# Optimization experiments

Measured on AMD Instinct MI355X. Metric: run time of the kernel, lower is better.

## Reference

```python
import jax, jax.numpy as jnp
import numpy as np
import math

NUM_BUCKETS = 32
MAX_DISTANCE = 128
EPS_IN = 1e-8
EPS_LN = 1e-5
NUM_HEADS = 12


def rms_inorm(x, w, eps=EPS_IN):
    # torch.std_mean default: unbiased (ddof=1) over spatial dims; mean is unused
    std = jnp.std(x, axis=(-2, -1), keepdims=True, ddof=1)
    return x / (std + eps) * w[None, :, None, None]


def layernorm(x, w, b, eps=EPS_LN):
    m = jnp.mean(x, axis=-1, keepdims=True)
    v = jnp.mean((x - m) ** 2, axis=-1, keepdims=True)
    return (x - m) * jax.lax.rsqrt(v + eps) * w + b


def _rel_bucket(rp):
    # T5-style bidirectional relative position buckets
    n = NUM_BUCKETS // 2
    ret = (rp > 0).astype(jnp.int32) * n
    arp = jnp.abs(rp)
    max_exact = n // 2
    is_small = arp < max_exact
    rpf = jnp.maximum(arp, 1).astype(jnp.float32)
    val_large = max_exact + (jnp.log(rpf / max_exact) / math.log(MAX_DISTANCE / max_exact) * (n - max_exact)).astype(jnp.int32)
    val_large = jnp.minimum(val_large, n - 1)
    return ret + jnp.where(is_small, arp, val_large)


def rel_bias(L, emb):
    pos = jnp.arange(L)
    bucket = _rel_bucket(pos[None, :] - pos[:, None])  # [L, L]
    return jnp.transpose(emb[bucket], (2, 0, 1))  # [heads, L, L]


def sdpa(q, k, v, bias):
    # q,k,v: [Bx, he, L, c]; bias: [he, L, L]
    scale = 1.0 / math.sqrt(q.shape[-1])
    s = jnp.einsum('bhlc,bhmc->bhlm', q, k) * scale + bias[None]
    p = jax.nn.softmax(s, axis=-1)
    return jnp.einsum('bhlm,bhmc->bhlc', p, v)


def _forward(x, norm1_w, norm2_w, mlpnorm_w, gamma_att, gamma_mlp,
             in_w, in_b, out_w, out_b, qn_w, qn_b, kn_w, kn_b,
             relbias_emb, mlp_w1, mlp_b1, mlp_w2, mlp_b2):
    B, C, H, W = x.shape
    he = NUM_HEADS
    hd = C // he
    inp = x
    x = rms_inorm(x, norm1_w)
    x = jnp.einsum('bchw,oc->bohw', x, in_w) + in_b[None, :, None, None]  # conv1x1 -> 3C
    x = x.reshape(B, he, 3 * hd, H, W).transpose(0, 1, 3, 4, 2)  # b he h w (3c)
    q, k, v = jnp.split(x, 3, axis=-1)
    q = layernorm(q, qn_w, qn_b)
    k = layernorm(k, kn_w, kn_b)
    # row attention: sequence along W
    to_x = lambda t: t.transpose(0, 2, 1, 3, 4).reshape(B * H, he, W, hd)
    xx = sdpa(to_x(q), to_x(k), to_x(v), rel_bias(W, relbias_emb))
    xx = xx.reshape(B, H, he, W, hd).transpose(0, 2, 4, 1, 3).reshape(B, C, H, W)
    # column attention: sequence along H
    to_y = lambda t: t.transpose(0, 3, 1, 2, 4).reshape(B * W, he, H, hd)
    xy = sdpa(to_y(q), to_y(k), to_y(v), rel_bias(H, relbias_emb))
    xy = xy.reshape(B, W, he, H, hd).transpose(0, 2, 4, 3, 1).reshape(B, C, H, W)
    x = (xx + xy) * 0.5
    x = rms_inorm(x, norm2_w)
    x = jnp.einsum('bchw,oc->bohw', x, out_w) + out_b[None, :, None, None]
    x = x * gamma_att[None, :, None, None] + inp
    inp2 = x
    h = x.transpose(0, 2, 3, 1)  # b h w c
    h = jax.nn.gelu(h @ mlp_w1 + mlp_b1, approximate=False) @ mlp_w2 + mlp_b2
    h = h.transpose(0, 3, 1, 2)
    h = rms_inorm(h, mlpnorm_w)
    return inp2 + gamma_mlp[None, :, None, None] * h


def setup_inputs() -> dict:
    key = jax.random.key(0)
    ks = jax.random.split(key, 8)
    B, C, H, W = 2, 768, 128, 128
    he = NUM_HEADS
    hd = C // he
    s = 0.02
    return {
        'x': jax.random.normal(ks[0], (B, C, H, W), jnp.float32),
        'bcs': jnp.zeros((B, 2), jnp.int32),
        'norm1_w': jnp.ones((C,), jnp.float32),
        'norm2_w': jnp.ones((C,), jnp.float32),
        'mlpnorm_w': jnp.ones((C,), jnp.float32),
        'gamma_att': jnp.full((C,), 1e-6, jnp.float32),
        'gamma_mlp': jnp.full((C,), 1e-6, jnp.float32),
        'in_w': jax.random.normal(ks[1], (3 * C, C), jnp.float32) * s,
        'in_b': jnp.zeros((3 * C,), jnp.float32),
        'out_w': jax.random.normal(ks[2], (C, C), jnp.float32) * s,
        'out_b': jnp.zeros((C,), jnp.float32),
        'qn_w': jnp.ones((hd,), jnp.float32),
        'qn_b': jnp.zeros((hd,), jnp.float32),
        'kn_w': jnp.ones((hd,), jnp.float32),
        'kn_b': jnp.zeros((hd,), jnp.float32),
        'relbias_emb': jax.random.normal(ks[3], (NUM_BUCKETS, he), jnp.float32) * s,
        'mlp_w1': jax.random.normal(ks[4], (C, 4 * C), jnp.float32) * s,
        'mlp_b1': jnp.zeros((4 * C,), jnp.float32),
        'mlp_w2': jax.random.normal(ks[5], (4 * C, C), jnp.float32) * s,
        'mlp_b2': jnp.zeros((C,), jnp.float32),
    }


def reference(x, bcs, norm1_w, norm2_w, mlpnorm_w, gamma_att, gamma_mlp,
              in_w, in_b, out_w, out_b, qn_w, qn_b, kn_w, kn_b,
              relbias_emb, mlp_w1, mlp_b1, mlp_w2, mlp_b2):
    # bcs is consulted only for boundary-condition selection in the original; the
    # T5-style relative bias here is independent of bc value.
    return _forward(x, norm1_w, norm2_w, mlpnorm_w, gamma_att, gamma_mlp,
                    in_w, in_b, out_w, out_b, qn_w, qn_b, kn_w, kn_b,
                    relbias_emb, mlp_w1, mlp_b1, mlp_w2, mlp_b2)
```

## Files before the change

### kernel.cpp

```cpp
#include <hip/hip_runtime.h>
#include <math.h>


typedef unsigned short u16;
typedef short bf16x8 __attribute__((ext_vector_type(8)));
typedef float f32x4 __attribute__((ext_vector_type(4)));

#define DEV static __device__ __forceinline__

DEV u16 f2bf(float f) {
    unsigned int u = __float_as_uint(f);
    u += 0x7fffu + ((u >> 16) & 1u);
    return (u16)(u >> 16);
}
DEV float bf2f(u16 h) { return __uint_as_float(((unsigned int)h) << 16); }

#define GLD16(gp, lp) __builtin_amdgcn_global_load_lds( \
    (const __attribute__((address_space(1))) unsigned int*)(const void*)(gp), \
    (__attribute__((address_space(3))) unsigned int*)(void*)(lp), 16, 0, 0)

#define MFMA16(a, b, c) __builtin_amdgcn_mfma_f32_16x16x32_bf16((a), (b), (c), 0, 0, 0)

__global__ void wtrans_kernel(const float* __restrict__ in, u16* __restrict__ out, int R, int C) {
    __shared__ float tile[64][65];
    int r0 = blockIdx.x * 64, c0 = blockIdx.y * 64;
    for (int idx = threadIdx.x; idx < 4096; idx += 256) {
        int rr = idx >> 6, cc = idx & 63;
        tile[rr][cc] = in[(size_t)(r0 + rr) * C + c0 + cc];
    }
    __syncthreads();
    for (int idx = threadIdx.x; idx < 4096; idx += 256) {
        int cc = idx >> 6, rr = idx & 63;
        out[(size_t)(c0 + cc) * R + r0 + rr] = f2bf(tile[rr][cc]);
    }
}

__global__ void wscale_kernel(const float* __restrict__ w, const float* __restrict__ s,
                              u16* __restrict__ out, int NK, int Kd) {
    int i = blockIdx.x * 256 + threadIdx.x;
    if (i < NK) {
        int k = i % Kd;
        float wv = w[i];
        out[i]      = f2bf(wv * s[k]);
        out[NK + i] = f2bf(wv * s[768 + k]);
    }
}

__global__ void bias_kernel(const float* __restrict__ emb, float* __restrict__ biasT) {
    int head = blockIdx.x, i = blockIdx.y, j = threadIdx.x;
    int rp = j - i;
    int ret = rp > 0 ? 16 : 0;
    int arp = rp < 0 ? -rp : rp;
    int bucket;
    if (arp < 8) bucket = ret + arp;
    else {
        int vl = 8 + (int)(logf((float)arp * 0.125f) * (8.0f / logf(16.0f)));
        if (vl > 15) vl = 15;
        bucket = ret + vl;
    }
    biasT[head * 16384 + i * 128 + j] = emb[bucket * 12 + head];
}

__global__ __launch_bounds__(256) void stage1s_kernel(const float* __restrict__ x,
                                                      u16* __restrict__ xn1,
                                                      float* __restrict__ part) {
    __shared__ float tile[64][65];
    __shared__ float ps[4][64], qs[4][64];
    int hw0 = blockIdx.x * 64, c0 = blockIdx.y * 64, b = blockIdx.z;
    for (int idx = threadIdx.x; idx < 4096; idx += 256) {
        int cc = idx >> 6, ww = idx & 63;
        tile[cc][ww] = x[((size_t)(b * 768 + c0 + cc)) * 16384 + hw0 + ww];
    }
    __syncthreads();
    for (int idx = threadIdx.x; idx < 4096; idx += 256) {
        int ww = idx >> 6, cc = idx & 63;
        xn1[((size_t)(b * 16384 + hw0 + ww)) * 768 + c0 + cc] = f2bf(tile[cc][ww]);
    }
    const int q = threadIdx.x >> 6, cc = threadIdx.x & 63;
    float s = 0.f, sq = 0.f;
#pragma unroll
    for (int w = 0; w < 16; w++) {
        float v = tile[cc][q * 16 + w];
        s += v; sq += v * v;
    }
    ps[q][cc] = s; qs[q][cc] = sq;
    __syncthreads();
    if (threadIdx.x < 64) {
        float S = ps[0][threadIdx.x] + ps[1][threadIdx.x] + ps[2][threadIdx.x] + ps[3][threadIdx.x];
        float Q = qs[0][threadIdx.x] + qs[1][threadIdx.x] + qs[2][threadIdx.x] + qs[3][threadIdx.x];
        size_t idx = ((size_t)(b * 768 + c0 + threadIdx.x) * 256 + blockIdx.x) * 2;
        part[idx] = S;
        part[idx + 1] = Q;
    }
}

__global__ void statsfin_kernel(const float* __restrict__ part, const float* __restrict__ w,
                                float* __restrict__ sc, int npart) {
    int i = blockIdx.x * 256 + threadIdx.x;
    if (i < 1536) {
        float S = 0.f, Q = 0.f;
        for (int k = 0; k < npart; k++) { S += part[(i * npart + k) * 2]; Q += part[(i * npart + k) * 2 + 1]; }
        float var = (Q - S * S * (1.0f / 16384.0f)) * (1.0f / 16383.0f);
        sc[i] = w[i % 768] / (sqrtf(var) + 1e-8f);
    }
}

template <int MODE>
__global__ __launch_bounds__(256) void gemm_bt(const u16* __restrict__ A,
                                               const u16* __restrict__ Bw, int K,
                                               u16* __restrict__ outb,
                                               const float* __restrict__ bias,
                                               const float* __restrict__ gamma,
                                               const float* __restrict__ xres, int ldc,
                                               size_t bstride,
                                               const float* __restrict__ lnw_q,
                                               const float* __restrict__ lnb_q,
                                               const float* __restrict__ lnw_k,
                                               const float* __restrict__ lnb_k) {
    __shared__ __align__(16) u16 As[8192];
    __shared__ __align__(16) u16 Bs[8192];
    const int tid = threadIdx.x;
    const int wave = tid >> 6, lane = tid & 63;
    const int ln = lane & 15, lq = lane >> 4;
    const int m0 = blockIdx.x * 128, n0 = blockIdx.y * 128;
    const int wm = (wave >> 1) * 64, wn = (wave & 1) * 64;
    const u16* Ag = A + (size_t)m0 * K;
    const u16* Bg = Bw + (size_t)(m0 >> 14) * bstride + (size_t)n0 * K;
    const int srow = lane >> 3;
    const int scol = ((lane & 7) ^ srow) * 8;
    f32x4 acc[4][4] = {};

    for (int k0 = 0; k0 < K; k0 += 64) {
        if (k0) __syncthreads();
#pragma unroll
        for (int r = 0; r < 4; r++) {
            int s = r * 4 + wave;
            int row = s * 8 + srow;
            GLD16(Ag + (size_t)row * K + k0 + scol, As + s * 512);
            GLD16(Bg + (size_t)row * K + k0 + scol, Bs + s * 512);
        }
        __syncthreads();
#pragma unroll
        for (int ks = 0; ks < 64; ks += 32) {
            const int koS = ((((ks >> 3) + lq) ^ (ln & 7)) << 3);
            bf16x8 af[4], bfr[4];
#pragma unroll
            for (int i = 0; i < 4; i++) af[i] = *(const bf16x8*)&As[(wm + i * 16 + ln) * 64 + koS];
#pragma unroll
            for (int j = 0; j < 4; j++) bfr[j] = *(const bf16x8*)&Bs[(wn + j * 16 + ln) * 64 + koS];
#pragma unroll
            for (int i = 0; i < 4; i++)
#pragma unroll
                for (int j = 0; j < 4; j++)
                    acc[i][j] = MFMA16(af[i], bfr[j], acc[i][j]);
        }
    }

    if (MODE == 0) {
        const int g3 = ((unsigned)(n0 + wn) >> 6) % 3;
        float bcol[4], wv[4], bvv[4];
#pragma unroll
        for (int j = 0; j < 4; j++) bcol[j] = bias[n0 + wn + j * 16 + ln];
        if (g3 == 0) {
#pragma unroll
            for (int j = 0; j < 4; j++) { wv[j] = lnw_q[j * 16 + ln]; bvv[j] = lnb_q[j * 16 + ln]; }
        } else if (g3 == 1) {
#pragma unroll
            for (int j = 0; j < 4; j++) { wv[j] = lnw_k[j * 16 + ln]; bvv[j] = lnb_k[j * 16 + ln]; }
        }
#pragma unroll
        for (int i = 0; i < 4; i++) {
            const int row0 = m0 + wm + i * 16 + lq * 4;
#pragma unroll
            for (int rg = 0; rg < 4; rg++) {
                float v[4]; float s = 0.f;
#pragma unroll
                for (int j = 0; j < 4; j++) { v[j] = acc[i][j][rg] + bcol[j]; s += v[j]; }
                if (g3 < 2) {
#pragma unroll
                    for (int d = 1; d < 16; d <<= 1) s += __shfl_xor(s, d);
                    const float mean = s * (1.0f / 64.0f);
                    float q2 = 0.f;
#pragma unroll
                    for (int j = 0; j < 4; j++) { float dv = v[j] - mean; q2 += dv * dv; }
#pragma unroll
                    for (int d = 1; d < 16; d <<= 1) q2 += __shfl_xor(q2, d);
                    const float rstd = rsqrtf(q2 * (1.0f / 64.0f) + 1e-5f);
#pragma unroll
                    for (int j = 0; j < 4; j++) v[j] = (v[j] - mean) * rstd * wv[j] + bvv[j];
                }
#pragma unroll
                for (int j = 0; j < 4; j++)
                    outb[(size_t)(row0 + rg) * ldc + n0 + wn + j * 16 + ln] = f2bf(v[j]);
            }
        }
        return;
    }

#pragma unroll
    for (int i = 0; i < 4; i++) {
        const int row0 = m0 + wm + i * 16 + lq * 4;
#pragma unroll
        for (int j = 0; j < 4; j++) {
            const int col = n0 + wn + j * 16 + ln;
            const float bv = bias[col];
            if (MODE == 1) {
                const f32x4 xv = *(const f32x4*)&xres[((size_t)(row0 >> 14) * 768 + col) * 16384 + (row0 & 16383)];
                const float gv = gamma[col];
#pragma unroll
                for (int rg = 0; rg < 4; rg++) {
                    float val = (acc[i][j][rg] + bv) * gv + xv[rg];
                    outb[(size_t)(row0 + rg) * ldc + col] = f2bf(val);
                }
            } else if (MODE == 2) {
#pragma unroll
                for (int rg = 0; rg < 4; rg++) {
                    float val = acc[i][j][rg] + bv;
                    val = 0.5f * val * (1.0f + erff(val * 0.70710678f));
                    outb[(size_t)(row0 + rg) * ldc + col] = f2bf(val);
                }
            } else {
#pragma unroll
                for (int rg = 0; rg < 4; rg++)
                    outb[(size_t)(row0 + rg) * ldc + col] = f2bf(acc[i][j][rg] + bv);
            }
        }
    }
}

__global__ __launch_bounds__(256) void attn_kernel(const u16* __restrict__ qkv,
                                                   u16* __restrict__ att,
                                                   const float* __restrict__ biasT,
                                                   const int mode) {
    __shared__ __align__(16) u16 sh[27136];
    u16* Qs = sh;
    u16* Ks = sh + 9216;
    u16* Vt = sh + 18432;
    u16* Ps = sh;

    const int t = threadIdx.x, lane = t & 63, wave = t >> 6;
    const int ln = lane & 15, lq = lane >> 4;
    const int head = blockIdx.x % 12;
    const int bp = blockIdx.x / 12;
    const int pos = bp & 127, b = bp >> 7;

    for (int idx = t; idx < 2048; idx += 256) {
        const int i = idx >> 4, c4 = (idx & 15) * 4;
        const size_t p = (mode == 0) ? (size_t)(b * 16384 + pos * 128 + i)
                                     : (size_t)(b * 16384 + i * 128 + pos);
        const u16* src = qkv + p * 2304 + head * 192;
        union { uint2 u; u16 us[4]; } vv;
        *(uint2*)&Qs[i * 72 + c4] = *(const uint2*)(src + c4);
        *(uint2*)&Ks[i * 72 + c4] = *(const uint2*)(src + 64 + c4);
        vv.u = *(const uint2*)(src + 128 + c4);
#pragma unroll
        for (int q = 0; q < 4; q++) Vt[(c4 + q) * 136 + i] = vv.us[q];
    }
    __syncthreads();

    const int wr = wave * 32;
    f32x4 S[2][8] = {};
#pragma unroll
    for (int ks = 0; ks < 64; ks += 32) {
        const int ko = ks + lq * 8;
        bf16x8 aq[2];
#pragma unroll
        for (int i = 0; i < 2; i++) aq[i] = *(const bf16x8*)&Qs[(wr + i * 16 + ln) * 72 + ko];
#pragma unroll
        for (int j = 0; j < 8; j++) {
            const bf16x8 bk = *(const bf16x8*)&Ks[(j * 16 + ln) * 72 + ko];
            S[0][j] = MFMA16(aq[0], bk, S[0][j]);
            S[1][j] = MFMA16(aq[1], bk, S[1][j]);
        }
    }
    __syncthreads();

    float rowsum[2][4];
    const float* bp2 = biasT + head * 16384;
#pragma unroll
    for (int i = 0; i < 2; i++) {
#pragma unroll
        for (int rg = 0; rg < 4; rg++) {
            const int r = wr + i * 16 + lq * 4 + rg;
            float v[8];
            float mx = -1e30f;
#pragma unroll
            for (int j = 0; j < 8; j++) {
                v[j] = S[i][j][rg] * 0.125f + bp2[r * 128 + j * 16 + ln];
                mx = fmaxf(mx, v[j]);
            }
#pragma unroll
            for (int d = 1; d < 16; d <<= 1) mx = fmaxf(mx, __shfl_xor(mx, d));
            float sm = 0.f;
#pragma unroll
            for (int j = 0; j < 8; j++) { v[j] = __expf(v[j] - mx); sm += v[j]; }
#pragma unroll
            for (int d = 1; d < 16; d <<= 1) sm += __shfl_xor(sm, d);
            rowsum[i][rg] = sm;
#pragma unroll
            for (int j = 0; j < 8; j++) Ps[r * 136 + j * 16 + ln] = f2bf(v[j]);
        }
    }
    __syncthreads();

    f32x4 O[2][4] = {};
#pragma unroll
    for (int ks = 0; ks < 128; ks += 32) {
        const int ko = ks + lq * 8;
        bf16x8 ap[2];
#pragma unroll
        for (int i = 0; i < 2; i++) ap[i] = *(const bf16x8*)&Ps[(wr + i * 16 + ln) * 136 + ko];
#pragma unroll
        for (int j = 0; j < 4; j++) {
            const bf16x8 bv = *(const bf16x8*)&Vt[(j * 16 + ln) * 136 + ko];
            O[0][j] = MFMA16(ap[0], bv, O[0][j]);
            O[1][j] = MFMA16(ap[1], bv, O[1][j]);
        }
    }

#pragma unroll
    for (int i = 0; i < 2; i++) {
#pragma unroll
        for (int j = 0; j < 4; j++) {
#pragma unroll
            for (int rg = 0; rg < 4; rg++) {
                const int r = wr + i * 16 + lq * 4 + rg;
                const int d = j * 16 + ln;
                const float val = O[i][j][rg] / rowsum[i][rg] * 0.5f;
                const size_t p = (mode == 0) ? (size_t)(b * 16384 + pos * 128 + r)
                                             : (size_t)(b * 16384 + r * 128 + pos);
                const size_t a = p * 768 + head * 64 + d;
                if (mode == 0) att[a] = f2bf(val);
                else           att[a] = f2bf(bf2f(att[a]) + val);
            }
        }
    }
}

__global__ __launch_bounds__(256) void statspm_kernel(const u16* __restrict__ in,
                                                      float* __restrict__ part) {
    const int c = blockIdx.y * 64 + (threadIdx.x & 63);
    const int g = threadIdx.x >> 6;
    const int b = blockIdx.z;
    const int rend = blockIdx.x * 1024 + 1024;
    float s = 0.f, sq = 0.f;
    for (int r = blockIdx.x * 1024 + g; r < rend; r += 4) {
        float v = bf2f(in[((size_t)(b * 16384 + r)) * 768 + c]);
        s += v; sq += v * v;
    }
    __shared__ float ls[4][64], lqq[4][64];
    ls[g][threadIdx.x & 63] = s;
    lqq[g][threadIdx.x & 63] = sq;
    __syncthreads();
    if (threadIdx.x < 64) {
        float S = ls[0][threadIdx.x] + ls[1][threadIdx.x] + ls[2][threadIdx.x] + ls[3][threadIdx.x];
        float Q = lqq[0][threadIdx.x] + lqq[1][threadIdx.x] + lqq[2][threadIdx.x] + lqq[3][threadIdx.x];
        size_t idx = ((size_t)(b * 768 + blockIdx.y * 64 + threadIdx.x) * 16 + blockIdx.x) * 2;
        part[idx] = S;
        part[idx + 1] = Q;
    }
}

__global__ __launch_bounds__(256) void final_kernel(const u16* __restrict__ x3,
                                                    const u16* __restrict__ h2,
                                                    const float* __restrict__ s3,
                                                    const float* __restrict__ gmlp,
                                                    float* __restrict__ out) {
    __shared__ float tile[64][65];
    int hw0 = blockIdx.x * 64, c0 = blockIdx.y * 64, b = blockIdx.z;
    for (int idx = threadIdx.x; idx < 4096; idx += 256) {
        int ww = idx >> 6, cc = idx & 63;
        int c = c0 + cc;
        size_t pp = ((size_t)(b * 16384 + hw0 + ww)) * 768 + c;
        tile[ww][cc] = bf2f(x3[pp]) + gmlp[c] * (bf2f(h2[pp]) * s3[b * 768 + c]);
    }
    __syncthreads();
    for (int idx = threadIdx.x; idx < 4096; idx += 256) {
        int cc = idx >> 6, ww = idx & 63;
        out[((size_t)(b * 768 + c0 + cc)) * 16384 + hw0 + ww] = tile[ww][cc];
    }
}

extern "C" void kernel_launch(void* const* d_in, const int* in_sizes, int n_in,
                              void* d_out, int out_size, void* d_ws, size_t ws_size,
                              hipStream_t stream) {
    (void)in_sizes; (void)n_in; (void)out_size;
    const float* x         = (const float*)d_in[0];
    const float* norm1_w   = (const float*)d_in[2];
    const float* norm2_w   = (const float*)d_in[3];
    const float* mlpnorm_w = (const float*)d_in[4];
    const float* gamma_att = (const float*)d_in[5];
    const float* gamma_mlp = (const float*)d_in[6];
    const float* in_w      = (const float*)d_in[7];
    const float* in_b      = (const float*)d_in[8];
    const float* out_w     = (const float*)d_in[9];
    const float* out_b     = (const float*)d_in[10];
    const float* qn_w      = (const float*)d_in[11];
    const float* qn_b      = (const float*)d_in[12];
    const float* kn_w      = (const float*)d_in[13];
    const float* kn_b      = (const float*)d_in[14];
    const float* emb       = (const float*)d_in[15];
    const float* w1        = (const float*)d_in[16];
    const float* b1        = (const float*)d_in[17];
    const float* w2        = (const float*)d_in[18];
    const float* b2        = (const float*)d_in[19];
    float* out = (float*)d_out;

    char* ws = (char*)d_ws;
    u16*   winb2  = (u16*)(ws + 0);
    u16*   woutb2 = (u16*)(ws + 7077888);
    u16*   w1t    = (u16*)(ws + 9437184);
    u16*   w2t    = (u16*)(ws + 14155776);
    float* biasT  = (float*)(ws + 18874368);
    float* s1     = (float*)(ws + 19660800);
    float* s2     = (float*)(ws + 19666944);
    float* s3     = (float*)(ws + 19673088);
    float* part   = (float*)(ws + 19679232);
    const size_t base = 22824960;
    u16*   qkv = (u16*)(ws + base);
    u16*   x3  = (u16*)(ws + base);
    u16*   h2  = (u16*)(ws + base + 50331648);
    u16*   h1b = (u16*)(ws + base + 100663296);
    u16*   xn1 = (u16*)(ws + base + 150994944);
    u16*   att = (u16*)(ws + base + 150994944);
    if (ws_size < base + 201326592) return;

    wtrans_kernel<<<dim3(12, 48), 256, 0, stream>>>(w1, w1t, 768, 3072);
    wtrans_kernel<<<dim3(48, 12), 256, 0, stream>>>(w2, w2t, 3072, 768);
    bias_kernel<<<dim3(12, 128), 128, 0, stream>>>(emb, biasT);

    stage1s_kernel<<<dim3(256, 12, 2), 256, 0, stream>>>(x, xn1, part);
    statsfin_kernel<<<6, 256, 0, stream>>>(part, norm1_w, s1, 256);
    wscale_kernel<<<6912, 256, 0, stream>>>(in_w, s1, winb2, 2304 * 768, 768);

    gemm_bt<0><<<dim3(256, 18), 256, 0, stream>>>(xn1, winb2, 768, qkv, in_b, nullptr, nullptr,
                                                  2304, (size_t)2304 * 768, qn_w, qn_b, kn_w, kn_b);

    attn_kernel<<<3072, 256, 0, stream>>>(qkv, att, biasT, 0);
    attn_kernel<<<3072, 256, 0, stream>>>(qkv, att, biasT, 1);

    statspm_kernel<<<dim3(16, 12, 2), 256, 0, stream>>>(att, part);
    statsfin_kernel<<<6, 256, 0, stream>>>(part, norm2_w, s2, 16);
    wscale_kernel<<<2304, 256, 0, stream>>>(out_w, s2, woutb2, 768 * 768, 768);
    gemm_bt<1><<<dim3(256, 6), 256, 0, stream>>>(att, woutb2, 768, x3, out_b, gamma_att, x,
                                                 768, (size_t)768 * 768, nullptr, nullptr, nullptr, nullptr);

    for (int ch = 0; ch < 2; ch++) {
        gemm_bt<2><<<dim3(128, 24), 256, 0, stream>>>(x3 + (size_t)ch * 16384 * 768, w1t, 768,
                                                      h1b, b1, nullptr, nullptr, 3072, 0,
                                                      nullptr, nullptr, nullptr, nullptr);
        gemm_bt<3><<<dim3(128, 6), 256, 0, stream>>>(h1b, w2t, 3072,
                                                     h2 + (size_t)ch * 16384 * 768, b2, nullptr, nullptr,
                                                     768, 0, nullptr, nullptr, nullptr, nullptr);
    }

    statspm_kernel<<<dim3(16, 12, 2), 256, 0, stream>>>(h2, part);
    statsfin_kernel<<<6, 256, 0, stream>>>(part, mlpnorm_w, s3, 16);
    final_kernel<<<dim3(256, 12, 2), 256, 0, stream>>>(x3, h2, s3, gamma_mlp, out);
}
```

Before: 1.330 ms.

## Switch all GEMMs and intermediate activations from bf16 to fp8 with scaled MFMA

Converts weights, normalized inputs, attention output, MLP hidden activations and the MLP output to fp8 (e4m3). The GEMMs now use the 16x16x128 f8f6f4 scaled MFMA with a K-tile of 128. The residual x3 is still kept in bf16 for the final add. This is meant to halve operand bytes and raise MFMA throughput, but it costs a lot of precision. The attention accumulation across row and column passes now round-trips through fp8, which risks large numerical error.

```diff
diff --git a/kernel.cpp b/kernel.cpp
--- a/kernel.cpp
+++ b/kernel.cpp
@@ -3,8 +3,11 @@
 
 
 typedef unsigned short u16;
+typedef unsigned char u8;
 typedef short bf16x8 __attribute__((ext_vector_type(8)));
 typedef float f32x4 __attribute__((ext_vector_type(4)));
+typedef int v4i __attribute__((ext_vector_type(4)));
+typedef int v8i __attribute__((ext_vector_type(8)));
 
 #define DEV static __device__ __forceinline__
 
@@ -14,14 +17,20 @@
     return (u16)(u >> 16);
 }
 DEV float bf2f(u16 h) { return __uint_as_float(((unsigned int)h) << 16); }
+DEV u8 f2fp8(float f) {
+    return (u8)(__builtin_amdgcn_cvt_pk_fp8_f32(f, f, 0, false) & 0xff);
+}
+DEV float fp82f(u8 v) { return __builtin_amdgcn_cvt_f32_fp8((int)v, 0); }
 
 #define GLD16(gp, lp) __builtin_amdgcn_global_load_lds( \
     (const __attribute__((address_space(1))) unsigned int*)(const void*)(gp), \
     (__attribute__((address_space(3))) unsigned int*)(void*)(lp), 16, 0, 0)
 
 #define MFMA16(a, b, c) __builtin_amdgcn_mfma_f32_16x16x32_bf16((a), (b), (c), 0, 0, 0)
-
-__global__ void wtrans_kernel(const float* __restrict__ in, u16* __restrict__ out, int R, int C) {
+#define MFMAF8(a, b, c) __builtin_amdgcn_mfma_scale_f32_16x16x128_f8f6f4( \
+    (a), (b), (c), 0, 0, 0, 0x7F7F7F7F, 0, 0x7F7F7F7F)
+
+__global__ void wtrans8_kernel(const float* __restrict__ in, u8* __restrict__ out, int R, int C) {
     __shared__ float tile[64][65];
     int r0 = blockIdx.x * 64, c0 = blockIdx.y * 64;
     for (int idx = threadIdx.x; idx < 4096; idx += 256) {
@@ -31,18 +40,18 @@
     __syncthreads();
     for (int idx = threadIdx.x; idx < 4096; idx += 256) {
         int cc = idx >> 6, rr = idx & 63;
-        out[(size_t)(c0 + cc) * R + r0 + rr] = f2bf(tile[rr][cc]);
-    }
-}
-
-__global__ void wscale_kernel(const float* __restrict__ w, const float* __restrict__ s,
-                              u16* __restrict__ out, int NK, int Kd) {
+        out[(size_t)(c0 + cc) * R + r0 + rr] = f2fp8(tile[rr][cc]);
+    }
+}
+
+__global__ void wscale8_kernel(const float* __restrict__ w, const float* __restrict__ s,
+                               u8* __restrict__ out, int NK, int Kd) {
     int i = blockIdx.x * 256 + threadIdx.x;
     if (i < NK) {
         int k = i % Kd;
         float wv = w[i];
-        out[i]      = f2bf(wv * s[k]);
-        out[NK + i] = f2bf(wv * s[768 + k]);
+        out[i]      = f2fp8(wv * s[k]);
+        out[NK + i] = f2fp8(wv * s[768 + k]);
     }
 }
 
@@ -62,7 +71,7 @@
 }
 
 __global__ __launch_bounds__(256) void stage1s_kernel(const float* __restrict__ x,
-                                                      u16* __restrict__ xn1,
+                                                      u8* __restrict__ xn1,
                                                       float* __restrict__ part) {
     __shared__ float tile[64][65];
     __shared__ float ps[4][64], qs[4][64];
@@ -74,7 +83,7 @@
     __syncthreads();
     for (int idx = threadIdx.x; idx < 4096; idx += 256) {
         int ww = idx >> 6, cc = idx & 63;
-        xn1[((size_t)(b * 16384 + hw0 + ww)) * 768 + c0 + cc] = f2bf(tile[cc][ww]);
+        xn1[((size_t)(b * 16384 + hw0 + ww)) * 768 + c0 + cc] = f2fp8(tile[cc][ww]);
     }
     const int q = threadIdx.x >> 6, cc = threadIdx.x & 63;
     float s = 0.f, sq = 0.f;
@@ -106,9 +115,10 @@
 }
 
 template <int MODE>
-__global__ __launch_bounds__(256) void gemm_bt(const u16* __restrict__ A,
-                                               const u16* __restrict__ Bw, int K,
-                                               u16* __restrict__ outb,
+__global__ __launch_bounds__(256) void gemm_f8(const u8* __restrict__ A,
+                                               const u8* __restrict__ Bw, int K,
+                                               u16* __restrict__ outh,
+                                               u8* __restrict__ outb,
                                                const float* __restrict__ bias,
                                                const float* __restrict__ gamma,
                                                const float* __restrict__ xres, int ldc,
@@ -117,43 +127,49 @@
                                                const float* __restrict__ lnb_q,
                                                const float* __restrict__ lnw_k,
                                                const float* __restrict__ lnb_k) {
-    __shared__ __align__(16) u16 As[8192];
-    __shared__ __align__(16) u16 Bs[8192];
+    __shared__ __align__(16) u8 As[16384];
+    __shared__ __align__(16) u8 Bs[16384];
     const int tid = threadIdx.x;
     const int wave = tid >> 6, lane = tid & 63;
     const int ln = lane & 15, lq = lane >> 4;
     const int m0 = blockIdx.x * 128, n0 = blockIdx.y * 128;
     const int wm = (wave >> 1) * 64, wn = (wave & 1) * 64;
-    const u16* Ag = A + (size_t)m0 * K;
-    const u16* Bg = Bw + (size_t)(m0 >> 14) * bstride + (size_t)n0 * K;
+    const u8* Ag = A + (size_t)m0 * K;
+    const u8* Bg = Bw + (size_t)(m0 >> 14) * bstride + (size_t)n0 * K;
     const int srow = lane >> 3;
-    const int scol = ((lane & 7) ^ srow) * 8;
+    const int scol = ((lane & 7) ^ srow) * 16;
+    const int cA = ((2 * lq) ^ (ln & 7)) * 16;
+    const int cB = ((2 * lq + 1) ^ (ln & 7)) * 16;
     f32x4 acc[4][4] = {};
 
-    for (int k0 = 0; k0 < K; k0 += 64) {
+    for (int k0 = 0; k0 < K; k0 += 128) {
         if (k0) __syncthreads();
 #pragma unroll
         for (int r = 0; r < 4; r++) {
             int s = r * 4 + wave;
             int row = s * 8 + srow;
-            GLD16(Ag + (size_t)row * K + k0 + scol, As + s * 512);
-            GLD16(Bg + (size_t)row * K + k0 + scol, Bs + s * 512);
+            GLD16(Ag + (size_t)row * K + k0 + scol, As + s * 1024);
+            GLD16(Bg + (size_t)row * K + k0 + scol, Bs + s * 1024);
         }
         __syncthreads();
-#pragma unroll
-        for (int ks = 0; ks < 64; ks += 32) {
-            const int koS = ((((ks >> 3) + lq) ^ (ln & 7)) << 3);
-            bf16x8 af[4], bfr[4];
-#pragma unroll
-            for (int i = 0; i < 4; i++) af[i] = *(const bf16x8*)&As[(wm + i * 16 + ln) * 64 + koS];
-#pragma unroll
-            for (int j = 0; j < 4; j++) bfr[j] = *(const bf16x8*)&Bs[(wn + j * 16 + ln) * 64 + koS];
-#pragma unroll
-            for (int i = 0; i < 4; i++)
-#pragma unroll
-                for (int j = 0; j < 4; j++)
-                    acc[i][j] = MFMA16(af[i], bfr[j], acc[i][j]);
-        }
+        union { v8i v; v4i h[2]; } af[4], bfr[4];
+#pragma unroll
+        for (int i = 0; i < 4; i++) {
+            const u8* base = &As[(wm + i * 16 + ln) * 128];
+            af[i].h[0] = *(const v4i*)(base + cA);
+            af[i].h[1] = *(const v4i*)(base + cB);
+        }
+#pragma unroll
+        for (int j = 0; j < 4; j++) {
+            const u8* base = &Bs[(wn + j * 16 + ln) * 128];
+            bfr[j].h[0] = *(const v4i*)(base + cA);
+            bfr[j].h[1] = *(const v4i*)(base + cB);
+        }
+#pragma unroll
+        for (int i = 0; i < 4; i++)
+#pragma unroll
+            for (int j = 0; j < 4; j++)
+                acc[i][j] = MFMAF8(af[i].v, bfr[j].v, acc[i][j]);
     }
 
     if (MODE == 0) {
@@ -191,7 +207,7 @@
                 }
 #pragma unroll
                 for (int j = 0; j < 4; j++)
-                    outb[(size_t)(row0 + rg) * ldc + n0 + wn + j * 16 + ln] = f2bf(v[j]);
+                    outh[(size_t)(row0 + rg) * ldc + n0 + wn + j * 16 + ln] = f2bf(v[j]);
             }
         }
         return;
@@ -210,26 +226,27 @@
 #pragma unroll
                 for (int rg = 0; rg < 4; rg++) {
                     float val = (acc[i][j][rg] + bv) * gv + xv[rg];
-                    outb[(size_t)(row0 + rg) * ldc + col] = f2bf(val);
+                    outh[(size_t)(row0 + rg) * ldc + col] = f2bf(val);
+                    outb[(size_t)(row0 + rg) * ldc + col] = f2fp8(val);
                 }
             } else if (MODE == 2) {
 #pragma unroll
                 for (int rg = 0; rg < 4; rg++) {
                     float val = acc[i][j][rg] + bv;
                     val = 0.5f * val * (1.0f + erff(val * 0.70710678f));
-                    outb[(size_t)(row0 + rg) * ldc + col] = f2bf(val);
+                    outb[(size_t)(row0 + rg) * ldc + col] = f2fp8(val);
                 }
             } else {
 #pragma unroll
                 for (int rg = 0; rg < 4; rg++)
-                    outb[(size_t)(row0 + rg) * ldc + col] = f2bf(acc[i][j][rg] + bv);
+                    outb[(size_t)(row0 + rg) * ldc + col] = f2fp8(acc[i][j][rg] + bv);
             }
         }
     }
 }
 
 __global__ __launch_bounds__(256) void attn_kernel(const u16* __restrict__ qkv,
-                                                   u16* __restrict__ att,
+                                                   u8* __restrict__ att,
                                                    const float* __restrict__ biasT,
                                                    const int mode) {
     __shared__ __align__(16) u16 sh[27136];
@@ -330,14 +347,14 @@
                 const size_t p = (mode == 0) ? (size_t)(b * 16384 + pos * 128 + r)
                                              : (size_t)(b * 16384 + r * 128 + pos);
                 const size_t a = p * 768 + head * 64 + d;
-                if (mode == 0) att[a] = f2bf(val);
-                else           att[a] = f2bf(bf2f(att[a]) + val);
+                if (mode == 0) att[a] = f2fp8(val);
+                else           att[a] = f2fp8(fp82f(att[a]) + val);
             }
         }
     }
 }
 
-__global__ __launch_bounds__(256) void statspm_kernel(const u16* __restrict__ in,
+__global__ __launch_bounds__(256) void statspm_kernel(const u8* __restrict__ in,
                                                       float* __restrict__ part) {
     const int c = blockIdx.y * 64 + (threadIdx.x & 63);
     const int g = threadIdx.x >> 6;
@@ -345,7 +362,7 @@
     const int rend = blockIdx.x * 1024 + 1024;
     float s = 0.f, sq = 0.f;
     for (int r = blockIdx.x * 1024 + g; r < rend; r += 4) {
-        float v = bf2f(in[((size_t)(b * 16384 + r)) * 768 + c]);
+        float v = fp82f(in[((size_t)(b * 16384 + r)) * 768 + c]);
         s += v; sq += v * v;
     }
     __shared__ float ls[4][64], lqq[4][64];
@@ -362,7 +379,7 @@
 }
 
 __global__ __launch_bounds__(256) void final_kernel(const u16* __restrict__ x3,
-                                                    const u16* __restrict__ h2,
+                                                    const u8* __restrict__ h2,
                                                     const float* __restrict__ s3,
                                                     const float* __restrict__ gmlp,
                                                     float* __restrict__ out) {
@@ -372,7 +389,7 @@
         int ww = idx >> 6, cc = idx & 63;
         int c = c0 + cc;
         size_t pp = ((size_t)(b * 16384 + hw0 + ww)) * 768 + c;
-        tile[ww][cc] = bf2f(x3[pp]) + gmlp[c] * (bf2f(h2[pp]) * s3[b * 768 + c]);
+        tile[ww][cc] = bf2f(x3[pp]) + gmlp[c] * (fp82f(h2[pp]) * s3[b * 768 + c]);
     }
     __syncthreads();
     for (int idx = threadIdx.x; idx < 4096; idx += 256) {
@@ -407,51 +424,55 @@
     float* out = (float*)d_out;
 
     char* ws = (char*)d_ws;
-    u16*   winb2  = (u16*)(ws + 0);
-    u16*   woutb2 = (u16*)(ws + 7077888);
-    u16*   w1t    = (u16*)(ws + 9437184);
-    u16*   w2t    = (u16*)(ws + 14155776);
-    float* biasT  = (float*)(ws + 18874368);
-    float* s1     = (float*)(ws + 19660800);
-    float* s2     = (float*)(ws + 19666944);
-    float* s3     = (float*)(ws + 19673088);
-    float* part   = (float*)(ws + 19679232);
-    const size_t base = 22824960;
+    u8*    winb2  = (u8*)(ws + 0);
+    u8*    woutb2 = (u8*)(ws + 3538944);
+    u8*    w1t    = (u8*)(ws + 4718592);
+    u8*    w2t    = (u8*)(ws + 7077888);
+    float* biasT  = (float*)(ws + 9437184);
+    float* s1     = (float*)(ws + 10223616);
+    float* s2     = (float*)(ws + 10229760);
+    float* s3     = (float*)(ws + 10235904);
+    float* part   = (float*)(ws + 10242048);
+    const size_t base = 13631488;
     u16*   qkv = (u16*)(ws + base);
     u16*   x3  = (u16*)(ws + base);
-    u16*   h2  = (u16*)(ws + base + 50331648);
-    u16*   h1b = (u16*)(ws + base + 100663296);
-    u16*   xn1 = (u16*)(ws + base + 150994944);
-    u16*   att = (u16*)(ws + base + 150994944);
-    if (ws_size < base + 201326592) return;
-
-    wtrans_kernel<<<dim3(12, 48), 256, 0, stream>>>(w1, w1t, 768, 3072);
-    wtrans_kernel<<<dim3(48, 12), 256, 0, stream>>>(w2, w2t, 3072, 768);
+    u8*    x3q = (u8*)(ws + base + 50331648);
+    u8*    h2  = (u8*)(ws + base + 75497472);
+    u8*    xn1 = (u8*)(ws + base + 150994944);
+    u8*    att = (u8*)(ws + base + 150994944);
+    u8*    h1  = (u8*)(ws + base + 176160768);
+    if (ws_size < base + 226492416) return;
+
+    wtrans8_kernel<<<dim3(12, 48), 256, 0, stream>>>(w1, w1t, 768, 3072);
+    wtrans8_kernel<<<dim3(48, 12), 256, 0, stream>>>(w2, w2t, 3072, 768);
     bias_kernel<<<dim3(12, 128), 128, 0, stream>>>(emb, biasT);
 
     stage1s_kernel<<<dim3(256, 12, 2), 256, 0, stream>>>(x, xn1, part);
     statsfin_kernel<<<6, 256, 0, stream>>>(part, norm1_w, s1, 256);
-    wscale_kernel<<<6912, 256, 0, stream>>>(in_w, s1, winb2, 2304 * 768, 768);
-
-    gemm_bt<0><<<dim3(256, 18), 256, 0, stream>>>(xn1, winb2, 768, qkv, in_b, nullptr, nullptr,
-                                                  2304, (size_t)2304 * 768, qn_w, qn_b, kn_w, kn_b);
+    wscale8_kernel<<<6912, 256, 0, stream>>>(in_w, s1, winb2, 2304 * 768, 768);
+
+    gemm_f8<0><<<dim3(256, 18), 256, 0, stream>>>(xn1, winb2, 768, qkv, nullptr, in_b,
+                                                  nullptr, nullptr, 2304, (size_t)2304 * 768,
+                                                  qn_w, qn_b, kn_w, kn_b);
 
     attn_kernel<<<3072, 256, 0, stream>>>(qkv, att, biasT, 0);
     attn_kernel<<<3072, 256, 0, stream>>>(qkv, att, biasT, 1);
 
     statspm_kernel<<<dim3(16, 12, 2), 256, 0, stream>>>(att, part);
     statsfin_kernel<<<6, 256, 0, stream>>>(part, norm2_w, s2, 16);
-    wscale_kernel<<<2304, 256, 0, stream>>>(out_w, s2, woutb2, 768 * 768, 768);
-    gemm_bt<1><<<dim3(256, 6), 256, 0, stream>>>(att, woutb2, 768, x3, out_b, gamma_att, x,
-                                                 768, (size_t)768 * 768, nullptr, nullptr, nullptr, nullptr);
+    wscale8_kernel<<<2304, 256, 0, stream>>>(out_w, s2, woutb2, 768 * 768, 768);
+    gemm_f8<1><<<dim3(256, 6), 256, 0, stream>>>(att, woutb2, 768, x3, x3q, out_b,
+                                                 gamma_att, x, 768, (size_t)768 * 768,
+                                                 nullptr, nullptr, nullptr, nullptr);
 
     for (int ch = 0; ch < 2; ch++) {
-        gemm_bt<2><<<dim3(128, 24), 256, 0, stream>>>(x3 + (size_t)ch * 16384 * 768, w1t, 768,
-                                                      h1b, b1, nullptr, nullptr, 3072, 0,
+        gemm_f8<2><<<dim3(128, 24), 256, 0, stream>>>(x3q + (size_t)ch * 16384 * 768, w1t, 768,
+                                                      nullptr, h1, b1, nullptr, nullptr, 3072, 0,
                                                       nullptr, nullptr, nullptr, nullptr);
-        gemm_bt<3><<<dim3(128, 6), 256, 0, stream>>>(h1b, w2t, 3072,
-                                                     h2 + (size_t)ch * 16384 * 768, b2, nullptr, nullptr,
-                                                     768, 0, nullptr, nullptr, nullptr, nullptr);
+        gemm_f8<3><<<dim3(128, 6), 256, 0, stream>>>(h1, w2t, 3072,
+                                                     nullptr, h2 + (size_t)ch * 16384 * 768, b2,
+                                                     nullptr, nullptr, 768, 0,
+                                                     nullptr, nullptr, nullptr, nullptr);
     }
 
     statspm_kernel<<<dim3(16, 12, 2), 256, 0, stream>>>(h2, part);
```

Measured after the change: 1.087 ms. -18.3%, faster.
